# Optimization experiments

Measured on AMD Instinct MI355X. Metric: run time of the kernel, lower is better.

Reference implementation:

```python
import jax, jax.numpy as jnp
import numpy as np

VOCAB, E, S, H, L = 32000, 1024, 2048, 16, 2
HS = E // H  # head_size = 64
EPS = 1e-5


def setup_inputs() -> dict:
    key = jax.random.key(0)
    ks = jax.random.split(key, 12)
    sc = 0.02
    inp = {
        "seq": jax.random.randint(ks[0], (S,), 0, VOCAB, dtype=jnp.int64)
        if jax.config.jax_enable_x64 else jax.random.randint(ks[0], (S,), 0, VOCAB, dtype=jnp.int32),
        "tok_emb": jax.random.normal(ks[1], (VOCAB, E), jnp.float32) * sc,
        "pos_emb": jax.random.normal(ks[2], (S, E), jnp.float32) * sc,
        "Wq": jax.random.normal(ks[3], (L, H, E, HS), jnp.float32) * sc,
        "Wk": jax.random.normal(ks[4], (L, H, E, HS), jnp.float32) * sc,
        "Wv": jax.random.normal(ks[5], (L, H, E, HS), jnp.float32) * sc,
        "Wr": jax.random.normal(ks[6], (L, E, E), jnp.float32) * sc,
        "br": jnp.zeros((L, E), jnp.float32),
        "W1": jax.random.normal(ks[7], (L, E, 4 * E), jnp.float32) * sc,
        "b1": jnp.zeros((L, 4 * E), jnp.float32),
        "W2": jax.random.normal(ks[8], (L, 4 * E, E), jnp.float32) * sc,
        "b2": jnp.zeros((L, E), jnp.float32),
        "ln_g": jnp.ones((L, E), jnp.float32),
        "ln_b": jnp.zeros((L, E), jnp.float32),
    }
    return inp


def _layer_norm(x, g, b):
    mu = jnp.mean(x, axis=-1, keepdims=True)
    var = jnp.mean(jnp.square(x - mu), axis=-1, keepdims=True)
    return (x - mu) * jax.lax.rsqrt(var + EPS) * g + b


def reference(seq, tok_emb, pos_emb, Wq, Wk, Wv, Wr, br, W1, b1, W2, b2, ln_g, ln_b):
    # embeddings: [S, E]
    x = tok_emb[seq] + pos_emb
    att_maps = []
    for l in range(L):
        # NOTE: the torch Block reuses the SAME LayerNorm instance twice per block.
        x = _layer_norm(x, ln_g[l], ln_b[l])
        # per-head projections: [H, S, HS]
        q = jnp.einsum('se,hed->hsd', x, Wq[l])
        k = jnp.einsum('se,hed->hsd', x, Wk[l])
        v = jnp.einsum('se,hed->hsd', x, Wv[l])
        # unmasked (encoder) attention, full [H, S, S] scores
        atts = jax.nn.softmax(jnp.einsum('hsd,htd->hst', q, k) / np.sqrt(HS), axis=-1)
        av = jnp.einsum('hst,htd->hsd', atts, v)  # [H, S, HS]
        cat = jnp.transpose(av, (1, 0, 2)).reshape(S, H * HS)  # concat heads -> [S, E]
        x = x + cat @ Wr[l] + br[l]
        x = _layer_norm(x, ln_g[l], ln_b[l])
        x = x + jax.nn.relu(x @ W1[l] + b1[l]) @ W2[l] + b2[l]
        att_maps.append(atts)
    return x, jnp.stack(att_maps)  # ([S,E], [L,H,S,S])
```

## Files before the change

### kernel.cpp

```cpp
#include <hip/hip_runtime.h>
#include <hip/hip_bf16.h>


constexpr int S_ = 2048;
constexpr int E_ = 1024;
constexpr int H_ = 16;
constexpr int HS_ = 64;
constexpr int L_ = 2;
constexpr int FF_ = 4096;

typedef __bf16 bf16;
typedef __bf16 bf16x8 __attribute__((ext_vector_type(8)));
typedef __bf16 bf16x4 __attribute__((ext_vector_type(4)));
typedef float f32x4 __attribute__((ext_vector_type(4)));

__device__ __forceinline__ void gld16(const void* g, const void* l) {
  __builtin_amdgcn_global_load_lds(
      (const __attribute__((address_space(1))) unsigned int*)g,
      (__attribute__((address_space(3))) unsigned int*)l, 16, 0, 0);
}

__global__ __launch_bounds__(256) void embed_ln_k(const int* __restrict__ seq,
                                                  const float* __restrict__ tok,
                                                  const float* __restrict__ pos,
                                                  const float* __restrict__ gw,
                                                  const float* __restrict__ bw,
                                                  float* __restrict__ x,
                                                  bf16* __restrict__ xb) {
  __shared__ float red[8];
  const int row = blockIdx.x, tid = threadIdx.x;
  const int t = seq[row];
  float4 v = ((const float4*)(tok + (long)t * E_))[tid];
  float4 p = ((const float4*)(pos + (long)row * E_))[tid];
  v.x += p.x; v.y += p.y; v.z += p.z; v.w += p.w;
  float s = v.x + v.y + v.z + v.w;
  float ss = v.x * v.x + v.y * v.y + v.z * v.z + v.w * v.w;
  for (int off = 32; off; off >>= 1) {
    s += __shfl_down(s, off);
    ss += __shfl_down(ss, off);
  }
  if ((tid & 63) == 0) { red[(tid >> 6) * 2] = s; red[(tid >> 6) * 2 + 1] = ss; }
  __syncthreads();
  if (tid == 0) {
    float S0 = 0, SS = 0;
    for (int i = 0; i < 4; ++i) { S0 += red[i * 2]; SS += red[i * 2 + 1]; }
    red[0] = S0; red[1] = SS;
  }
  __syncthreads();
  const float mu = red[0] * (1.f / E_);
  const float var = red[1] * (1.f / E_) - mu * mu;
  const float rs = rsqrtf(var + 1e-5f);
  float4 gv = ((const float4*)gw)[tid], bv = ((const float4*)bw)[tid];
  float4 o;
  o.x = (v.x - mu) * rs * gv.x + bv.x;
  o.y = (v.y - mu) * rs * gv.y + bv.y;
  o.z = (v.z - mu) * rs * gv.z + bv.z;
  o.w = (v.w - mu) * rs * gv.w + bv.w;
  ((float4*)(x + (long)row * E_))[tid] = o;
  bf16x4 ob;
  ob[0] = (__bf16)o.x; ob[1] = (__bf16)o.y; ob[2] = (__bf16)o.z; ob[3] = (__bf16)o.w;
  ((bf16x4*)(xb + (long)row * E_))[tid] = ob;
}

__global__ __launch_bounds__(256) void layernorm_k(float* __restrict__ x,
                                                   const float* __restrict__ gw,
                                                   const float* __restrict__ bw,
                                                   bf16* __restrict__ xb) {
  __shared__ float red[8];
  const int row = blockIdx.x, tid = threadIdx.x;
  float4 v = ((const float4*)(x + (long)row * E_))[tid];
  float s = v.x + v.y + v.z + v.w;
  float ss = v.x * v.x + v.y * v.y + v.z * v.z + v.w * v.w;
  for (int off = 32; off; off >>= 1) {
    s += __shfl_down(s, off);
    ss += __shfl_down(ss, off);
  }
  if ((tid & 63) == 0) { red[(tid >> 6) * 2] = s; red[(tid >> 6) * 2 + 1] = ss; }
  __syncthreads();
  if (tid == 0) {
    float S0 = 0, SS = 0;
    for (int i = 0; i < 4; ++i) { S0 += red[i * 2]; SS += red[i * 2 + 1]; }
    red[0] = S0; red[1] = SS;
  }
  __syncthreads();
  const float mu = red[0] * (1.f / E_);
  const float var = red[1] * (1.f / E_) - mu * mu;
  const float rs = rsqrtf(var + 1e-5f);
  float4 gv = ((const float4*)gw)[tid], bv = ((const float4*)bw)[tid];
  float4 o;
  o.x = (v.x - mu) * rs * gv.x + bv.x;
  o.y = (v.y - mu) * rs * gv.y + bv.y;
  o.z = (v.z - mu) * rs * gv.z + bv.z;
  o.w = (v.w - mu) * rs * gv.w + bv.w;
  ((float4*)(x + (long)row * E_))[tid] = o;
  bf16x4 ob;
  ob[0] = (__bf16)o.x; ob[1] = (__bf16)o.y; ob[2] = (__bf16)o.z; ob[3] = (__bf16)o.w;
  ((bf16x4*)(xb + (long)row * E_))[tid] = ob;
}

__global__ __launch_bounds__(256) void repack_k(const float* __restrict__ wq,
                                                const float* __restrict__ wk,
                                                const float* __restrict__ wv,
                                                const float* __restrict__ wr,
                                                const float* __restrict__ w1,
                                                const float* __restrict__ w2,
                                                bf16* __restrict__ qkvT,
                                                bf16* __restrict__ wrT,
                                                bf16* __restrict__ w1T,
                                                bf16* __restrict__ w2T) {
  __shared__ float t[32][33];
  const int tx = threadIdx.x, ty = threadIdx.y;
  const int bid = blockIdx.x;
  const float* src;
  bf16* dst;
  long ld_in, ld_out, r0, c0;
  if (bid < 3072) {
    const int j = bid >> 10;
    const int z = (bid & 1023) >> 6;
    const int rem = bid & 63;
    r0 = (rem >> 1) * 32;
    c0 = (rem & 1) * 32;
    const float* w = j == 0 ? wq : (j == 1 ? wk : wv);
    src = w + (long)z * E_ * HS_;
    dst = qkvT + (long)j * E_ * E_ + (long)z * HS_ * E_;
    ld_in = HS_; ld_out = E_;
  } else if (bid < 4096) {
    const int idx = bid - 3072;
    r0 = (idx >> 5) * 32; c0 = (idx & 31) * 32;
    src = wr; dst = wrT; ld_in = E_; ld_out = E_;
  } else if (bid < 8192) {
    const int idx = bid - 4096;
    r0 = (idx >> 7) * 32; c0 = (idx & 127) * 32;
    src = w1; dst = w1T; ld_in = FF_; ld_out = E_;
  } else {
    const int idx = bid - 8192;
    r0 = (idx >> 5) * 32; c0 = (idx & 31) * 32;
    src = w2; dst = w2T; ld_in = E_; ld_out = FF_;
  }
#pragma unroll
  for (int i = 0; i < 4; ++i)
    t[ty + 8 * i][tx] = src[(r0 + ty + 8 * i) * ld_in + c0 + tx];
  __syncthreads();
#pragma unroll
  for (int i = 0; i < 4; ++i)
    dst[(c0 + ty + 8 * i) * ld_out + r0 + tx] = (__bf16)t[tx][ty + 8 * i];
}

__global__ __launch_bounds__(256) void trans_b2b(const bf16* __restrict__ in,
                                                 bf16* __restrict__ out,
                                                 long ld_in, long ld_out) {
  __shared__ bf16 t[32][33];
  const int tx = threadIdx.x, ty = threadIdx.y;
  const long r0 = (long)blockIdx.x * 32, c0 = (long)blockIdx.y * 32;
#pragma unroll
  for (int i = 0; i < 4; ++i)
    t[ty + 8 * i][tx] = in[(r0 + ty + 8 * i) * ld_in + c0 + tx];
  __syncthreads();
#pragma unroll
  for (int i = 0; i < 4; ++i)
    out[(c0 + ty + 8 * i) * ld_out + r0 + tx] = t[tx][ty + 8 * i];
}

template <int WM, int WN>
__global__ __launch_bounds__(WM * WN * 64) void gemm_lds(
    const bf16* __restrict__ A, const bf16* __restrict__ B,
    long lda, long ldb, int K, int mtiles, float scale,
    const float* __restrict__ bias, const float* __restrict__ resid, int relu,
    float* __restrict__ Cf, long ldc, bf16* __restrict__ Cb, long ldcb) {
  constexpr int BM = WM * 64, BN = WN * 64, NW = WM * WN;
  constexpr int ABYTES = BM * 64;
  constexpr int BUFB = ABYTES + BN * 64;
  constexpr int NCH = BUFB / 1024;
  constexpr int CPT = NCH / NW;
  static_assert(CPT == 4 || CPT == 6, "unexpected CPT");
  __shared__ char smem[3 * BUFB];

  const int tid = threadIdx.x, wid = tid >> 6, lane = tid & 63;
  const int cpx = gridDim.x >> 3;
  const int bid = blockIdx.x;
  const int wg = (bid & 7) * cpx + (bid >> 3);
  const long m0 = (long)(wg % mtiles) * BM;
  const long n0 = (long)(wg / mtiles) * BN;

  const char* gsrc[CPT];
  int ldsbase[CPT];
#pragma unroll
  for (int i = 0; i < CPT; ++i) {
    const int c = wid + i * NW;
    const int s = c * 1024 + lane * 16;
    const bf16* base;
    int kb;
    if (s < ABYTES) {
      const int row = s >> 6;
      kb = (s ^ ((row & 3) << 4)) & 63;
      base = A + (m0 + row) * lda;
    } else {
      const int s2 = s - ABYTES;
      const int row = s2 >> 6;
      kb = (s2 ^ ((row & 3) << 4)) & 63;
      base = B + (n0 + row) * ldb;
    }
    gsrc[i] = (const char*)base + kb;
    ldsbase[i] = c * 1024;
  }

  const int fr = lane & 15, fg = lane >> 4;
  const int wm = wid % WM, wn = wid / WM;
  int aoff[4], boff[4];
#pragma unroll
  for (int t = 0; t < 4; ++t) {
    const int m = wm * 64 + t * 16 + fr;
    aoff[t] = m * 64 + ((16 * fg) ^ ((m & 3) << 4));
    const int n = wn * 64 + t * 16 + fr;
    boff[t] = ABYTES + n * 64 + ((16 * fg) ^ ((n & 3) << 4));
  }

  f32x4 acc[4][4];
#pragma unroll
  for (int i = 0; i < 4; ++i)
#pragma unroll
    for (int j = 0; j < 4; ++j) acc[i][j] = (f32x4){0.f, 0.f, 0.f, 0.f};

  const int nt = K >> 5;

  auto stage = [&](int tile, int buf) {
    const long koff = (long)tile * 64;
#pragma unroll
    for (int i = 0; i < CPT; ++i)
      gld16(gsrc[i] + koff, smem + buf * BUFB + ldsbase[i]);
  };

  stage(0, 0);
  stage(1, 1);

  int cur = 0;
  for (int t = 0; t < nt; ++t) {
    if (t < nt - 1) {
      if constexpr (CPT == 4) asm volatile("s_waitcnt vmcnt(4)" ::: "memory");
      else asm volatile("s_waitcnt vmcnt(6)" ::: "memory");
    } else {
      asm volatile("s_waitcnt vmcnt(0)" ::: "memory");
    }
    __builtin_amdgcn_s_barrier();
    if (t + 2 < nt) {
      int sb = cur + 2; if (sb >= 3) sb -= 3;
      stage(t + 2, sb);
    }
    const char* sbuf = smem + cur * BUFB;
    bf16x8 a[4], b[4];
#pragma unroll
    for (int i = 0; i < 4; ++i) a[i] = *(const bf16x8*)(sbuf + aoff[i]);
#pragma unroll
    for (int i = 0; i < 4; ++i) b[i] = *(const bf16x8*)(sbuf + boff[i]);
#pragma unroll
    for (int i = 0; i < 4; ++i)
#pragma unroll
      for (int j = 0; j < 4; ++j)
        acc[i][j] = __builtin_amdgcn_mfma_f32_16x16x32_bf16(a[i], b[j], acc[i][j], 0, 0, 0);
    cur = cur + 1; if (cur >= 3) cur -= 3;
  }

#pragma unroll
  for (int tm = 0; tm < 4; ++tm) {
#pragma unroll
    for (int tn = 0; tn < 4; ++tn) {
      const long col = n0 + wn * 64 + tn * 16 + fr;
#pragma unroll
      for (int i = 0; i < 4; ++i) {
        const long row = m0 + wm * 64 + tm * 16 + fg * 4 + i;
        float v = acc[tm][tn][i] * scale;
        if (bias) v += bias[col];
        if (relu) v = v > 0.f ? v : 0.f;
        if (resid) v += resid[row * ldc + col];
        if (Cf) Cf[row * ldc + col] = v;
        if (Cb) Cb[row * ldcb + col] = (__bf16)v;
      }
    }
  }
}

__global__ __launch_bounds__(256, 2) void gemm_ksplit(
    const bf16* __restrict__ A, const bf16* __restrict__ B,
    long lda, long ldb, int K, int mtiles, float scale,
    const float* __restrict__ bias, const float* __restrict__ resid, int relu,
    float* __restrict__ Cf, long ldc, bf16* __restrict__ Cb, long ldcb) {
  __shared__ char smem[4 * 16384];

  const int tid = threadIdx.x, w = tid >> 6, lane = tid & 63;
  const int cpx = gridDim.x >> 3;
  const int bid = blockIdx.x;
  const int wg = (bid & 7) * cpx + (bid >> 3);
  const long m0 = (long)(wg % mtiles) * 64;
  const long n0 = (long)(wg / mtiles) * 64;
  const int Kq = K >> 2;
  const long k0w = (long)w * Kq;

  const char* gsrc[8];
  int ldsoff[8];
#pragma unroll
  for (int i = 0; i < 8; ++i) {
    const int s = (i & 3) * 1024 + lane * 16;
    const int row = s >> 6;
    const int kb = (s ^ ((row & 3) << 4)) & 63;
    const bf16* base = (i < 4) ? (A + (m0 + row) * lda + k0w)
                               : (B + (n0 + row) * ldb + k0w);
    gsrc[i] = (const char*)base + kb;
    ldsoff[i] = w * 16384 + i * 1024;
  }

  const int fr = lane & 15, fg = lane >> 4;
  int aoff[4], boff[4];
#pragma unroll
  for (int t = 0; t < 4; ++t) {
    const int m = t * 16 + fr;
    aoff[t] = w * 16384 + m * 64 + ((16 * fg) ^ ((m & 3) << 4));
    boff[t] = aoff[t] + 4096;
  }

  f32x4 acc[4][4];
#pragma unroll
  for (int i = 0; i < 4; ++i)
#pragma unroll
    for (int j = 0; j < 4; ++j) acc[i][j] = (f32x4){0.f, 0.f, 0.f, 0.f};

  const int nt = Kq >> 5;

  auto stage = [&](int tile, int buf) {
    const long koff = (long)tile * 64;
#pragma unroll
    for (int i = 0; i < 8; ++i)
      gld16(gsrc[i] + koff, smem + ldsoff[i] + buf * 8192);
  };

  stage(0, 0);
  if (nt > 1) stage(1, 1);

  for (int t = 0; t < nt; ++t) {
    if (t + 1 < nt) asm volatile("s_waitcnt vmcnt(8)" ::: "memory");
    else asm volatile("s_waitcnt vmcnt(0)" ::: "memory");
    const int bsel = (t & 1) * 8192;
    bf16x8 a[4], b[4];
#pragma unroll
    for (int i = 0; i < 4; ++i) a[i] = *(const bf16x8*)(smem + aoff[i] + bsel);
#pragma unroll
    for (int i = 0; i < 4; ++i) b[i] = *(const bf16x8*)(smem + boff[i] + bsel);
#pragma unroll
    for (int i = 0; i < 4; ++i)
#pragma unroll
      for (int j = 0; j < 4; ++j)
        acc[i][j] = __builtin_amdgcn_mfma_f32_16x16x32_bf16(a[i], b[j], acc[i][j], 0, 0, 0);
    if (t + 2 < nt) stage(t + 2, t & 1);
  }

  __syncthreads();
#pragma unroll
  for (int f = 0; f < 16; ++f)
    *(f32x4*)(smem + w * 16384 + f * 1024 + lane * 16) = acc[f >> 2][f & 3];
  __syncthreads();

#pragma unroll
  for (int tn = 0; tn < 4; ++tn) {
    const int f = w * 4 + tn;
    f32x4 v0 = *(const f32x4*)(smem + 0 * 16384 + f * 1024 + lane * 16);
    f32x4 v1 = *(const f32x4*)(smem + 1 * 16384 + f * 1024 + lane * 16);
    f32x4 v2 = *(const f32x4*)(smem + 2 * 16384 + f * 1024 + lane * 16);
    f32x4 v3 = *(const f32x4*)(smem + 3 * 16384 + f * 1024 + lane * 16);
    f32x4 sv;
#pragma unroll
    for (int i = 0; i < 4; ++i) sv[i] = v0[i] + v1[i] + v2[i] + v3[i];
    const long col = n0 + tn * 16 + fr;
#pragma unroll
    for (int i = 0; i < 4; ++i) {
      const long row = m0 + w * 16 + fg * 4 + i;
      float v = sv[i] * scale;
      if (bias) v += bias[col];
      if (relu) v = v > 0.f ? v : 0.f;
      if (resid) v += resid[row * ldc + col];
      if (Cf) Cf[row * ldc + col] = v;
      if (Cb) Cb[row * ldcb + col] = (__bf16)v;
    }
  }
}

__global__ __launch_bounds__(256, 2) void attn_fused(
    const bf16* __restrict__ qkv,
    const bf16* __restrict__ vt,
    float* __restrict__ att,
    bf16* __restrict__ avb) {
  constexpr int QB = 64, KB = 128;
  constexpr int NKT = S_ / KB;
  constexpr float C2 = 0.1803368801111244f;
  __shared__ char plds[QB * 256];

  const int tid = threadIdx.x, lane = tid & 63, w = tid >> 6;
  const int fr = lane & 15, fg = lane >> 4;
  const int bid = blockIdx.x;
  const int wg = (bid & 7) * 64 + (bid >> 3);
  const int h = wg >> 5;
  const long q0 = (long)(wg & 31) * QB;
  const int q = w * 16 + fr;
  const int swz = (q & 15) << 4;

  bf16x8 qf[2];
#pragma unroll
  for (int k0 = 0; k0 < 2; ++k0)
    qf[k0] = *(const bf16x8*)(qkv + (q0 + q) * (3 * E_) + h * HS_ + k0 * 32 + fg * 8);

  float l_ = 0.f;

  for (int kt = 0; kt < NKT; ++kt) {
    const long t0 = (long)kt * KB;
    bf16x8 kf[8][2];
#pragma unroll
    for (int mt = 0; mt < 8; ++mt)
#pragma unroll
      for (int k0 = 0; k0 < 2; ++k0)
        kf[mt][k0] = *(const bf16x8*)(qkv + (t0 + mt * 16 + fr) * (3 * E_) +
                                      E_ + h * HS_ + k0 * 32 + fg * 8);
    f32x4 acc[8];
#pragma unroll
    for (int mt = 0; mt < 8; ++mt) acc[mt] = (f32x4){0.f, 0.f, 0.f, 0.f};
#pragma unroll
    for (int k0 = 0; k0 < 2; ++k0)
#pragma unroll
      for (int mt = 0; mt < 8; ++mt)
        acc[mt] = __builtin_amdgcn_mfma_f32_16x16x32_bf16(kf[mt][k0], qf[k0], acc[mt], 0, 0, 0);
    float sum = 0.f;
#pragma unroll
    for (int mt = 0; mt < 8; ++mt)
#pragma unroll
      for (int i = 0; i < 4; ++i) sum += __builtin_amdgcn_exp2f(acc[mt][i] * C2);
    l_ += sum;
  }
  l_ += __shfl_xor(l_, 16);
  l_ += __shfl_xor(l_, 32);
  const float li = -__log2f(l_);

  f32x4 ao[4];
#pragma unroll
  for (int d = 0; d < 4; ++d) ao[d] = (f32x4){0.f, 0.f, 0.f, 0.f};

  for (int kt = 0; kt < NKT; ++kt) {
    const long t0 = (long)kt * KB;
    bf16x8 kf[8][2];
#pragma unroll
    for (int mt = 0; mt < 8; ++mt)
#pragma unroll
      for (int k0 = 0; k0 < 2; ++k0)
        kf[mt][k0] = *(const bf16x8*)(qkv + (t0 + mt * 16 + fr) * (3 * E_) +
                                      E_ + h * HS_ + k0 * 32 + fg * 8);
    f32x4 acc[8];
#pragma unroll
    for (int mt = 0; mt < 8; ++mt) acc[mt] = (f32x4){0.f, 0.f, 0.f, 0.f};
#pragma unroll
    for (int k0 = 0; k0 < 2; ++k0)
#pragma unroll
      for (int mt = 0; mt < 8; ++mt)
        acc[mt] = __builtin_amdgcn_mfma_f32_16x16x32_bf16(kf[mt][k0], qf[k0], acc[mt], 0, 0, 0);

    float* arow = att + ((long)h * S_ + q0 + q) * S_ + t0;
#pragma unroll
    for (int mt = 0; mt < 8; ++mt) {
      f32x4 pv;
#pragma unroll
      for (int i = 0; i < 4; ++i)
        pv[i] = __builtin_amdgcn_exp2f(fmaf(acc[mt][i], C2, li));
      __builtin_nontemporal_store(pv, (f32x4*)(arow + mt * 16 + fg * 4));
      bf16x4 pb;
      pb[0] = (__bf16)pv[0]; pb[1] = (__bf16)pv[1];
      pb[2] = (__bf16)pv[2]; pb[3] = (__bf16)pv[3];
      const int tb = (mt * 16 + fg * 4) * 2;
      *(bf16x4*)(plds + q * 256 + ((tb & ~15) ^ swz) + (tb & 15)) = pb;
    }

#pragma unroll
    for (int k0 = 0; k0 < 4; ++k0) {
      const bf16x8 bq = *(const bf16x8*)(plds + q * 256 + ((k0 * 64 + fg * 16) ^ swz));
#pragma unroll
      for (int dmt = 0; dmt < 4; ++dmt) {
        bf16x8 av = *(const bf16x8*)(vt + (long)(h * HS_ + dmt * 16 + fr) * S_ +
                                     t0 + k0 * 32 + fg * 8);
        ao[dmt] = __builtin_amdgcn_mfma_f32_16x16x32_bf16(av, bq, ao[dmt], 0, 0, 0);
      }
    }
  }

#pragma unroll
  for (int dmt = 0; dmt < 4; ++dmt) {
    bf16x4 o;
    o[0] = (__bf16)ao[dmt][0]; o[1] = (__bf16)ao[dmt][1];
    o[2] = (__bf16)ao[dmt][2]; o[3] = (__bf16)ao[dmt][3];
    *(bf16x4*)(avb + (q0 + q) * E_ + h * HS_ + dmt * 16 + fg * 4) = o;
  }
}

extern "C" void kernel_launch(void* const* d_in, const int* in_sizes, int n_in,
                              void* d_out, int out_size, void* d_ws, size_t ws_size,
                              hipStream_t stream) {
  const int* seq = (const int*)d_in[0];
  const float* tok_emb = (const float*)d_in[1];
  const float* pos_emb = (const float*)d_in[2];
  const float* Wq = (const float*)d_in[3];
  const float* Wk = (const float*)d_in[4];
  const float* Wv = (const float*)d_in[5];
  const float* Wr = (const float*)d_in[6];
  const float* br = (const float*)d_in[7];
  const float* W1 = (const float*)d_in[8];
  const float* b1 = (const float*)d_in[9];
  const float* W2 = (const float*)d_in[10];
  const float* b2 = (const float*)d_in[11];
  const float* ln_g = (const float*)d_in[12];
  const float* ln_b = (const float*)d_in[13];

  float* outx = (float*)d_out;
  float* att_all = outx + (long)S_ * E_;

  char* w = (char*)d_ws;
  auto alloc = [&](size_t bytes) {
    char* p = w;
    w += (bytes + 255) & ~(size_t)255;
    return p;
  };
  float* x = (float*)alloc((size_t)S_ * E_ * 4);
  bf16* xb = (bf16*)alloc((size_t)S_ * E_ * 2);
  bf16* qkvb = (bf16*)alloc((size_t)S_ * 3 * E_ * 2);
  bf16* vt = (bf16*)alloc((size_t)E_ * S_ * 2);
  bf16* avb = (bf16*)alloc((size_t)S_ * E_ * 2);
  bf16* hb = (bf16*)alloc((size_t)S_ * FF_ * 2);
  bf16* wqkvT = (bf16*)alloc((size_t)3 * E_ * E_ * 2);
  bf16* wrT = (bf16*)alloc((size_t)E_ * E_ * 2);
  bf16* w1T = (bf16*)alloc((size_t)E_ * FF_ * 2);
  bf16* w2T = (bf16*)alloc((size_t)E_ * FF_ * 2);
  (void)ws_size; (void)in_sizes; (void)n_in; (void)out_size;

  embed_ln_k<<<S_, 256, 0, stream>>>(seq, tok_emb, pos_emb, ln_g, ln_b, x, xb);

  for (int l = 0; l < L_; ++l) {
    repack_k<<<12288, dim3(32, 8, 1), 0, stream>>>(
        Wq + (long)l * H_ * E_ * HS_, Wk + (long)l * H_ * E_ * HS_,
        Wv + (long)l * H_ * E_ * HS_, Wr + (long)l * E_ * E_,
        W1 + (long)l * E_ * FF_, W2 + (long)l * FF_ * E_,
        wqkvT, wrT, w1T, w2T);

    if (l > 0)
      layernorm_k<<<S_, 256, 0, stream>>>(x, ln_g + (long)l * E_, ln_b + (long)l * E_, xb);

    gemm_lds<2, 2><<<dim3(16 * 24), 256, 0, stream>>>(
        xb, wqkvT, E_, E_, E_, 16, 1.f, nullptr, nullptr, 0,
        nullptr, 0, qkvb, 3 * E_);

    trans_b2b<<<dim3(S_ / 32, E_ / 32, 1), dim3(32, 8, 1), 0, stream>>>(
        qkvb + 2 * E_, vt, 3 * E_, S_);

    float* att_l = att_all + (long)l * H_ * S_ * S_;
    attn_fused<<<512, 256, 0, stream>>>(qkvb, vt, att_l, avb);

    gemm_ksplit<<<32 * 16, 256, 0, stream>>>(
        avb, wrT, E_, E_, E_, 32, 1.f, br + (long)l * E_, x, 0,
        x, E_, nullptr, 0);

    layernorm_k<<<S_, 256, 0, stream>>>(x, ln_g + (long)l * E_, ln_b + (long)l * E_, xb);

    gemm_lds<2, 2><<<dim3(16 * 32), 256, 0, stream>>>(
        xb, w1T, E_, E_, E_, 16, 1.f, b1 + (long)l * FF_, nullptr, 1,
        nullptr, 0, hb, FF_);

    float* xdst = (l == L_ - 1) ? outx : x;
    gemm_ksplit<<<32 * 16, 256, 0, stream>>>(
        hb, w2T, FF_, FF_, FF_, 32, 1.f, b2 + (long)l * E_, x, 0,
        xdst, E_, nullptr, 0);
  }
}
```

Baseline: 699.6 us.

## Replace shared-tile GEMM with per-wave private LDS tiles and no barriers

Replaces the 2x2-wave GEMM that shares a 128x128 LDS tile across four waves with a 2-wave kernel in which each wave stages its own 64x64 A and B tiles into a private LDS region, double-buffered. Because no wave reads another wave's LDS data, the per-iteration workgroup barrier is dropped and each wave only waits on its own vmcnt. The cost is lower data reuse: A rows are loaded separately by both waves and the block tile is smaller, which roughly doubles global/L2 traffic per FLOP and doubles the grid size. The double buffer also prefetches only one tile ahead, down from two.

```diff
diff --git a/kernel.cpp b/kernel.cpp
--- a/kernel.cpp
+++ b/kernel.cpp
@@ -161,58 +161,40 @@
     out[(c0 + ty + 8 * i) * ld_out + r0 + tx] = t[tx][ty + 8 * i];
 }
 
-template <int WM, int WN>
-__global__ __launch_bounds__(WM * WN * 64) void gemm_lds(
+__global__ __launch_bounds__(128) void gemm_bf2(
     const bf16* __restrict__ A, const bf16* __restrict__ B,
     long lda, long ldb, int K, int mtiles, float scale,
     const float* __restrict__ bias, const float* __restrict__ resid, int relu,
     float* __restrict__ Cf, long ldc, bf16* __restrict__ Cb, long ldcb) {
-  constexpr int BM = WM * 64, BN = WN * 64, NW = WM * WN;
-  constexpr int ABYTES = BM * 64;
-  constexpr int BUFB = ABYTES + BN * 64;
-  constexpr int NCH = BUFB / 1024;
-  constexpr int CPT = NCH / NW;
-  static_assert(CPT == 4 || CPT == 6, "unexpected CPT");
-  __shared__ char smem[3 * BUFB];
-
-  const int tid = threadIdx.x, wid = tid >> 6, lane = tid & 63;
+  __shared__ char smem[2 * 16384];
+
+  const int tid = threadIdx.x, w = tid >> 6, lane = tid & 63;
   const int cpx = gridDim.x >> 3;
   const int bid = blockIdx.x;
   const int wg = (bid & 7) * cpx + (bid >> 3);
-  const long m0 = (long)(wg % mtiles) * BM;
-  const long n0 = (long)(wg / mtiles) * BN;
-
-  const char* gsrc[CPT];
-  int ldsbase[CPT];
-#pragma unroll
-  for (int i = 0; i < CPT; ++i) {
-    const int c = wid + i * NW;
-    const int s = c * 1024 + lane * 16;
-    const bf16* base;
-    int kb;
-    if (s < ABYTES) {
-      const int row = s >> 6;
-      kb = (s ^ ((row & 3) << 4)) & 63;
-      base = A + (m0 + row) * lda;
-    } else {
-      const int s2 = s - ABYTES;
-      const int row = s2 >> 6;
-      kb = (s2 ^ ((row & 3) << 4)) & 63;
-      base = B + (n0 + row) * ldb;
-    }
+  const long m0 = (long)(wg % mtiles) * 64;
+  const long n0 = (long)(wg / mtiles) * 128 + w * 64;
+
+  const char* gsrc[8];
+  int ldsoff[8];
+#pragma unroll
+  for (int i = 0; i < 8; ++i) {
+    const int s = (i & 3) * 1024 + lane * 16;
+    const int row = s >> 6;
+    const int kb = (s ^ ((row & 3) << 4)) & 63;
+    const bf16* base = (i < 4) ? (A + (m0 + row) * lda)
+                               : (B + (n0 + row) * ldb);
     gsrc[i] = (const char*)base + kb;
-    ldsbase[i] = c * 1024;
+    ldsoff[i] = w * 16384 + i * 1024;
   }
 
   const int fr = lane & 15, fg = lane >> 4;
-  const int wm = wid % WM, wn = wid / WM;
   int aoff[4], boff[4];
 #pragma unroll
   for (int t = 0; t < 4; ++t) {
-    const int m = wm * 64 + t * 16 + fr;
-    aoff[t] = m * 64 + ((16 * fg) ^ ((m & 3) << 4));
-    const int n = wn * 64 + t * 16 + fr;
-    boff[t] = ABYTES + n * 64 + ((16 * fg) ^ ((n & 3) << 4));
+    const int m = t * 16 + fr;
+    aoff[t] = w * 16384 + m * 64 + ((16 * fg) ^ ((m & 3) << 4));
+    boff[t] = aoff[t] + 4096;
   }
 
   f32x4 acc[4][4];
@@ -226,48 +208,38 @@
   auto stage = [&](int tile, int buf) {
     const long koff = (long)tile * 64;
 #pragma unroll
-    for (int i = 0; i < CPT; ++i)
-      gld16(gsrc[i] + koff, smem + buf * BUFB + ldsbase[i]);
+    for (int i = 0; i < 8; ++i)
+      gld16(gsrc[i] + koff, smem + ldsoff[i] + buf * 8192);
   };
 
   stage(0, 0);
-  stage(1, 1);
-
-  int cur = 0;
+  if (nt > 1) stage(1, 1);
+
   for (int t = 0; t < nt; ++t) {
-    if (t < nt - 1) {
-      if constexpr (CPT == 4) asm volatile("s_waitcnt vmcnt(4)" ::: "memory");
-      else asm volatile("s_waitcnt vmcnt(6)" ::: "memory");
-    } else {
-      asm volatile("s_waitcnt vmcnt(0)" ::: "memory");
-    }
-    __builtin_amdgcn_s_barrier();
-    if (t + 2 < nt) {
-      int sb = cur + 2; if (sb >= 3) sb -= 3;
-      stage(t + 2, sb);
-    }
-    const char* sbuf = smem + cur * BUFB;
+    if (t + 1 < nt) asm volatile("s_waitcnt vmcnt(8)" ::: "memory");
+    else asm volatile("s_waitcnt vmcnt(0)" ::: "memory");
+    const int bsel = (t & 1) * 8192;
     bf16x8 a[4], b[4];
 #pragma unroll
-    for (int i = 0; i < 4; ++i) a[i] = *(const bf16x8*)(sbuf + aoff[i]);
-#pragma unroll
-    for (int i = 0; i < 4; ++i) b[i] = *(const bf16x8*)(sbuf + boff[i]);
+    for (int i = 0; i < 4; ++i) a[i] = *(const bf16x8*)(smem + aoff[i] + bsel);
+#pragma unroll
+    for (int i = 0; i < 4; ++i) b[i] = *(const bf16x8*)(smem + boff[i] + bsel);
 #pragma unroll
     for (int i = 0; i < 4; ++i)
 #pragma unroll
       for (int j = 0; j < 4; ++j)
         acc[i][j] = __builtin_amdgcn_mfma_f32_16x16x32_bf16(a[i], b[j], acc[i][j], 0, 0, 0);
-    cur = cur + 1; if (cur >= 3) cur -= 3;
+    if (t + 2 < nt) stage(t + 2, t & 1);
   }
 
 #pragma unroll
   for (int tm = 0; tm < 4; ++tm) {
 #pragma unroll
     for (int tn = 0; tn < 4; ++tn) {
-      const long col = n0 + wn * 64 + tn * 16 + fr;
+      const long col = n0 + tn * 16 + fr;
 #pragma unroll
       for (int i = 0; i < 4; ++i) {
-        const long row = m0 + wm * 64 + tm * 16 + fg * 4 + i;
+        const long row = m0 + tm * 16 + fg * 4 + i;
         float v = acc[tm][tn][i] * scale;
         if (bias) v += bias[col];
         if (relu) v = v > 0.f ? v : 0.f;
@@ -545,8 +517,8 @@
     if (l > 0)
       layernorm_k<<<S_, 256, 0, stream>>>(x, ln_g + (long)l * E_, ln_b + (long)l * E_, xb);
 
-    gemm_lds<2, 2><<<dim3(16 * 24), 256, 0, stream>>>(
-        xb, wqkvT, E_, E_, E_, 16, 1.f, nullptr, nullptr, 0,
+    gemm_bf2<<<768, 128, 0, stream>>>(
+        xb, wqkvT, E_, E_, E_, 32, 1.f, nullptr, nullptr, 0,
         nullptr, 0, qkvb, 3 * E_);
 
     trans_b2b<<<dim3(S_ / 32, E_ / 32, 1), dim3(32, 8, 1), 0, stream>>>(
@@ -561,8 +533,8 @@
 
     layernorm_k<<<S_, 256, 0, stream>>>(x, ln_g + (long)l * E_, ln_b + (long)l * E_, xb);
 
-    gemm_lds<2, 2><<<dim3(16 * 32), 256, 0, stream>>>(
-        xb, w1T, E_, E_, E_, 16, 1.f, b1 + (long)l * FF_, nullptr, 1,
+    gemm_bf2<<<1024, 128, 0, stream>>>(
+        xb, w1T, E_, E_, E_, 32, 1.f, b1 + (long)l * FF_, nullptr, 1,
         nullptr, 0, hb, FF_);
 
     float* xdst = (l == L_ - 1) ? outx : x;
```

Result: slower. 727.8 us (+4.0%).
